# Kernel tuning notes

Measured on AMD Instinct MI355X. Metric: run time of the kernel, lower is better.

Reference implementation:

```python
import jax, jax.numpy as jnp
import numpy as np

N_NODES = 100000


def gcn_conv(x, edge_index, W, b, n_nodes):
    # GCNConv: out = D^{-1/2} (A + I) D^{-1/2} X W + b  (add_self_loops=True)
    xw = x @ W  # [N, F_out]
    loop = jnp.arange(n_nodes, dtype=edge_index.dtype)
    row = jnp.concatenate([edge_index[0], loop])  # source
    col = jnp.concatenate([edge_index[1], loop])  # target
    ones = jnp.ones(row.shape[0], dtype=x.dtype)
    deg = jax.ops.segment_sum(ones, col, num_segments=n_nodes)
    dinv = jnp.where(deg > 0, jax.lax.rsqrt(deg), 0.0)
    norm = dinv[row] * dinv[col]  # [E+N]
    msgs = norm[:, None] * xw[row]  # gather + scale
    out = jax.ops.segment_sum(msgs, col, num_segments=n_nodes)  # scatter-add
    return out + b


def setup_inputs() -> dict:
    key = jax.random.key(0)
    k1, k2, k3, k4 = jax.random.split(key, 4)
    x = jax.random.normal(k1, (N_NODES, 512), dtype=jnp.float32)
    edge_index = jax.random.randint(k2, (2, 3200000), 0, N_NODES, dtype=jnp.int64)
    W1 = jax.random.normal(k3, (512, 16), dtype=jnp.float32) * (1.0 / np.sqrt(512))
    b1 = jnp.zeros((16,), dtype=jnp.float32)
    W2 = jax.random.normal(k4, (16, 7), dtype=jnp.float32) * (1.0 / np.sqrt(16))
    b2 = jnp.zeros((7,), dtype=jnp.float32)
    return {"x": x, "edge_index": edge_index, "W1": W1, "b1": b1, "W2": W2, "b2": b2}


def reference(x, edge_index, W1, b1, W2, b2):
    n = x.shape[0]
    h = gcn_conv(x, edge_index, W1, b1, n)
    h = jax.nn.relu(h)
    # F.dropout(training=self.training) is identity in eval mode
    h = gcn_conv(h, edge_index, W2, b2, n)
    return jax.nn.log_softmax(h, axis=1)
```

## Files before the change

### kernel.cpp

```cpp
#include <hip/hip_runtime.h>
#include <math.h>
#include <stdint.h>

#define NBMAX 512
#define BCAP 10240

__device__ __forceinline__ unsigned int f2bf(float f) {
    unsigned int u = __float_as_uint(f);
    return (u + 0x7FFFu + ((u >> 16) & 1u)) >> 16;
}
__device__ __forceinline__ float bl(unsigned int u) { return __uint_as_float(u << 16); }
__device__ __forceinline__ float bh(unsigned int u) { return __uint_as_float(u & 0xFFFF0000u); }

__global__ void k_zero(int* __restrict__ p, int n) {
    int i = threadIdx.x;
    if (i < n) p[i] = 0;
}

__global__ __launch_bounds__(256) void k_hist_gemm(
    const int* __restrict__ col, int* __restrict__ bucketCnt, int E, int hB, int NB,
    const float* __restrict__ x, const float* __restrict__ W1,
    float* __restrict__ xw, int n) {
    __shared__ float4 sW[2048];
    __shared__ int histL[NBMAX];
    if (blockIdx.x < hB) {
        for (int t = threadIdx.x; t < NB; t += 256) histL[t] = 0;
        __syncthreads();
        int base = blockIdx.x * 4096;
#pragma unroll
        for (int i = 0; i < 16; ++i) {
            int e = base + threadIdx.x + i * 256;
            if (e < E) atomicAdd(&histL[col[e] >> 8], 1);
        }
        __syncthreads();
        for (int t = threadIdx.x; t < NB; t += 256) {
            int c = histL[t];
            if (c) atomicAdd(&bucketCnt[t], c);
        }
        return;
    }
    const float4* w4 = (const float4*)W1;
    for (int p = threadIdx.x; p < 2048; p += 256) sW[p] = w4[p];
    __syncthreads();

    int idx  = (blockIdx.x - hB) * 256 + threadIdx.x;
    int node = idx >> 2, q = idx & 3;
    if (node >= n) return;

    const float4* xr = (const float4*)(x + (size_t)node * 512);
    float ax = 0.f, ay = 0.f, az = 0.f, aw = 0.f;
#pragma unroll 4
    for (int kk = 0; kk < 128; ++kk) {
        float4 xv  = xr[kk];
        float4 w0  = sW[(4 * kk + 0) * 4 + q];
        float4 w1v = sW[(4 * kk + 1) * 4 + q];
        float4 w2v = sW[(4 * kk + 2) * 4 + q];
        float4 w3v = sW[(4 * kk + 3) * 4 + q];
        ax = fmaf(xv.x, w0.x, ax);  ay = fmaf(xv.x, w0.y, ay);
        az = fmaf(xv.x, w0.z, az);  aw = fmaf(xv.x, w0.w, aw);
        ax = fmaf(xv.y, w1v.x, ax); ay = fmaf(xv.y, w1v.y, ay);
        az = fmaf(xv.y, w1v.z, az); aw = fmaf(xv.y, w1v.w, aw);
        ax = fmaf(xv.z, w2v.x, ax); ay = fmaf(xv.z, w2v.y, ay);
        az = fmaf(xv.z, w2v.z, az); aw = fmaf(xv.z, w2v.w, aw);
        ax = fmaf(xv.w, w3v.x, ax); ay = fmaf(xv.w, w3v.y, ay);
        az = fmaf(xv.w, w3v.z, az); aw = fmaf(xv.w, w3v.w, aw);
    }
    float4 r; r.x = ax; r.y = ay; r.z = az; r.w = aw;
    ((float4*)xw)[idx] = r;
}

__global__ void k_scanB(const int* __restrict__ bucketCnt, int* __restrict__ baseB,
                        int* __restrict__ cursor, int* __restrict__ offs,
                        int NB, int N, int E) {
    __shared__ int s[512];
    int t = threadIdx.x;
    int c = (t < NB) ? bucketCnt[t] : 0;
    s[t] = c;
    __syncthreads();
    for (int o = 1; o < 512; o <<= 1) {
        int v = (t >= o) ? s[t - o] : 0;
        __syncthreads();
        s[t] += v;
        __syncthreads();
    }
    if (t < NB) { int ex = s[t] - c; baseB[t] = ex; cursor[t] = ex; }
    if (t == NB) baseB[NB] = E;
    if (t == 0) offs[N] = E;
}

__global__ __launch_bounds__(512) void k_bucket(
    const int* __restrict__ row, const int* __restrict__ col,
    int* __restrict__ cursor, unsigned int* __restrict__ sortedG, int E, int NB) {
    __shared__ int histL[NBMAX];
    __shared__ int offsL[NBMAX];
    __shared__ int gbL[NBMAX];
    __shared__ int sbuf[512];
    __shared__ unsigned int stageW[4096];
    __shared__ unsigned short stageB[4096];
    int t = threadIdx.x;
    for (int i = t; i < NB; i += 512) histL[i] = 0;
    __syncthreads();
    int off = blockIdx.x * 4096;
    unsigned int w[8]; int bk[8]; int rk[8];
#pragma unroll
    for (int i = 0; i < 8; ++i) {
        int e = off + t + i * 512;
        if (e < E) {
            int c = col[e], r = row[e];
            w[i]  = ((unsigned int)r << 8) | (unsigned int)(c & 255);
            bk[i] = c >> 8;
            rk[i] = atomicAdd(&histL[bk[i]], 1);
        } else bk[i] = -1;
    }
    __syncthreads();
    int cnt = (t < NB) ? histL[t] : 0;
    sbuf[t] = cnt;
    __syncthreads();
    for (int o = 1; o < 512; o <<= 1) {
        int v = (t >= o) ? sbuf[t - o] : 0;
        __syncthreads();
        sbuf[t] += v;
        __syncthreads();
    }
    if (t < NB) {
        offsL[t] = sbuf[t] - cnt;
        gbL[t]   = cnt ? atomicAdd(&cursor[t], cnt) : 0;
    }
    __syncthreads();
#pragma unroll
    for (int i = 0; i < 8; ++i) {
        if (bk[i] >= 0) {
            int s2 = offsL[bk[i]] + rk[i];
            stageW[s2] = w[i];
            stageB[s2] = (unsigned short)bk[i];
        }
    }
    __syncthreads();
    int total = min(4096, E - off);
    for (int s2 = t; s2 < total; s2 += 512) {
        int b = stageB[s2];
        sortedG[gbL[b] + (s2 - offsL[b])] = stageW[s2];
    }
}

__global__ __launch_bounds__(512) void k_sortscale(
    unsigned int* __restrict__ sortedG, const int* __restrict__ baseB,
    int* __restrict__ offs, float* __restrict__ dinv,
    const float* __restrict__ xw, unsigned int* __restrict__ sxwh, int N) {
    __shared__ unsigned int wv[BCAP];
    __shared__ int hist[256];
    __shared__ int off_[256];
    __shared__ int sc[256];
    __shared__ float ds[256];
    int t = threadIdx.x, b = blockIdx.x;
    if (t < 256) hist[t] = 0;
    __syncthreads();
    int beg = baseB[b], end = baseB[b + 1];
    int cnt = end - beg;
    for (int i = t; i < cnt; i += 512) {
        unsigned int w = sortedG[beg + i];
        wv[i] = w;
        atomicAdd(&hist[w & 255], 1);
    }
    __syncthreads();
    if (t < 256) sc[t] = hist[t];
    __syncthreads();
    for (int o = 1; o < 256; o <<= 1) {
        int v = 0;
        if (t < 256 && t >= o) v = sc[t - o];
        __syncthreads();
        if (t < 256) sc[t] += v;
        __syncthreads();
    }
    if (t < 256) {
        off_[t] = sc[t] - hist[t];
        int node = b * 256 + t;
        float dv = rsqrtf((float)(hist[t] + 1));
        ds[t] = dv;
        if (node < N) { offs[node] = beg + off_[t]; dinv[node] = dv; }
        hist[t] = 0;
    }
    __syncthreads();
    for (int i = t; i < cnt; i += 512) {
        unsigned int w = wv[i];
        int c = w & 255;
        int r2 = atomicAdd(&hist[c], 1);
        sortedG[beg + off_[c] + r2] = w >> 8;
    }
    const float4* xw4 = (const float4*)xw;
    uint2* dsth = (uint2*)sxwh;
#pragma unroll
    for (int k = 0; k < 2; ++k) {
        int idx = t + k * 512;
        int nl  = idx >> 2;
        int node = b * 256 + nl;
        if (node < N) {
            float s = ds[nl];
            float4 v = xw4[(size_t)b * 1024 + idx];
            unsigned int u0 = f2bf(v.x * s), u1 = f2bf(v.y * s);
            unsigned int u2 = f2bf(v.z * s), u3 = f2bf(v.w * s);
            uint2 o; o.x = u0 | (u1 << 16); o.y = u2 | (u3 << 16);
            dsth[(size_t)b * 1024 + idx] = o;
        }
    }
}

__global__ __launch_bounds__(256) void k_gather1f(
    const int* __restrict__ offs, const int* __restrict__ srow,
    const uint4* __restrict__ s4, const float* __restrict__ dinv,
    const float* __restrict__ W2, const float* __restrict__ b1,
    float* __restrict__ sxw2p, int N) {
    __shared__ float sW2[112];
    __shared__ float sb1[16];
    if (threadIdx.x < 112) sW2[threadIdx.x] = W2[threadIdx.x];
    if (threadIdx.x < 16) sb1[threadIdx.x] = b1[threadIdx.x];
    __syncthreads();
    int idx = blockIdx.x * 256 + threadIdx.x;
    int node = idx >> 1, q = idx & 1;
    if (node >= N) return;
    int beg = offs[node], end = offs[node + 1];

    uint4 sv = s4[(size_t)node * 2 + q];
    float a0 = bl(sv.x), a1 = bh(sv.x), a2 = bl(sv.y), a3 = bh(sv.y);
    float a4 = bl(sv.z), a5 = bh(sv.z), a6 = bl(sv.w), a7 = bh(sv.w);
    int j = beg;
    for (; j + 3 < end; j += 4) {
        int r0 = srow[j], r1 = srow[j + 1], r2 = srow[j + 2], r3 = srow[j + 3];
        uint4 v0 = s4[(size_t)r0 * 2 + q];
        uint4 v1 = s4[(size_t)r1 * 2 + q];
        uint4 v2 = s4[(size_t)r2 * 2 + q];
        uint4 v3 = s4[(size_t)r3 * 2 + q];
        a0 += (bl(v0.x) + bl(v1.x)) + (bl(v2.x) + bl(v3.x));
        a1 += (bh(v0.x) + bh(v1.x)) + (bh(v2.x) + bh(v3.x));
        a2 += (bl(v0.y) + bl(v1.y)) + (bl(v2.y) + bl(v3.y));
        a3 += (bh(v0.y) + bh(v1.y)) + (bh(v2.y) + bh(v3.y));
        a4 += (bl(v0.z) + bl(v1.z)) + (bl(v2.z) + bl(v3.z));
        a5 += (bh(v0.z) + bh(v1.z)) + (bh(v2.z) + bh(v3.z));
        a6 += (bl(v0.w) + bl(v1.w)) + (bl(v2.w) + bl(v3.w));
        a7 += (bh(v0.w) + bh(v1.w)) + (bh(v2.w) + bh(v3.w));
    }
    for (; j < end; ++j) {
        int r = srow[j];
        uint4 v = s4[(size_t)r * 2 + q];
        a0 += bl(v.x); a1 += bh(v.x); a2 += bl(v.y); a3 += bh(v.y);
        a4 += bl(v.z); a5 += bh(v.z); a6 += bl(v.w); a7 += bh(v.w);
    }
    float d = dinv[node];
    float h[8];
    h[0] = fmaxf(fmaf(d, a0, sb1[q * 8 + 0]), 0.f);
    h[1] = fmaxf(fmaf(d, a1, sb1[q * 8 + 1]), 0.f);
    h[2] = fmaxf(fmaf(d, a2, sb1[q * 8 + 2]), 0.f);
    h[3] = fmaxf(fmaf(d, a3, sb1[q * 8 + 3]), 0.f);
    h[4] = fmaxf(fmaf(d, a4, sb1[q * 8 + 4]), 0.f);
    h[5] = fmaxf(fmaf(d, a5, sb1[q * 8 + 5]), 0.f);
    h[6] = fmaxf(fmaf(d, a6, sb1[q * 8 + 6]), 0.f);
    h[7] = fmaxf(fmaf(d, a7, sb1[q * 8 + 7]), 0.f);
    float o[7] = {0.f, 0.f, 0.f, 0.f, 0.f, 0.f, 0.f};
    int rbase = q * 8;
#pragma unroll
    for (int i = 0; i < 8; ++i) {
        float hv = h[i];
#pragma unroll
        for (int jj = 0; jj < 7; ++jj) o[jj] = fmaf(hv, sW2[(rbase + i) * 7 + jj], o[jj]);
    }
#pragma unroll
    for (int jj = 0; jj < 7; ++jj) o[jj] += __shfl_xor(o[jj], 1, 64);
    float4 wv4;
    if (q == 0) { wv4.x = o[0] * d; wv4.y = o[1] * d; wv4.z = o[2] * d; wv4.w = o[3] * d; }
    else        { wv4.x = o[4] * d; wv4.y = o[5] * d; wv4.z = o[6] * d; wv4.w = 0.f; }
    ((float4*)sxw2p)[(size_t)node * 2 + q] = wv4;
}

__global__ __launch_bounds__(256) void k_gather2f(
    const int* __restrict__ offs, const int* __restrict__ srow,
    const float* __restrict__ sxw2p, const float* __restrict__ dinv,
    const float* __restrict__ b2, float* __restrict__ out, int N) {
    __shared__ float sb2[8];
    if (threadIdx.x < 7) sb2[threadIdx.x] = b2[threadIdx.x];
    if (threadIdx.x == 7) sb2[7] = 0.f;
    __syncthreads();
    int idx = blockIdx.x * 256 + threadIdx.x;
    int node = idx >> 1, q = idx & 1;
    if (node >= N) return;
    int beg = offs[node], end = offs[node + 1];
    const float4* s4 = (const float4*)sxw2p;
    float4 a = s4[(size_t)node * 2 + q];
    int j = beg;
    for (; j + 3 < end; j += 4) {
        int r0 = srow[j], r1 = srow[j + 1], r2 = srow[j + 2], r3 = srow[j + 3];
        float4 v0 = s4[(size_t)r0 * 2 + q];
        float4 v1 = s4[(size_t)r1 * 2 + q];
        float4 v2 = s4[(size_t)r2 * 2 + q];
        float4 v3 = s4[(size_t)r3 * 2 + q];
        a.x += (v0.x + v1.x) + (v2.x + v3.x);
        a.y += (v0.y + v1.y) + (v2.y + v3.y);
        a.z += (v0.z + v1.z) + (v2.z + v3.z);
        a.w += (v0.w + v1.w) + (v2.w + v3.w);
    }
    for (; j < end; ++j) {
        int r = srow[j];
        float4 v = s4[(size_t)r * 2 + q];
        a.x += v.x; a.y += v.y; a.z += v.z; a.w += v.w;
    }
    float d = dinv[node];
    float z0 = fmaf(d, a.x, sb2[q * 4 + 0]);
    float z1 = fmaf(d, a.y, sb2[q * 4 + 1]);
    float z2 = fmaf(d, a.z, sb2[q * 4 + 2]);
    float z3 = (q == 0) ? fmaf(d, a.w, sb2[3]) : -INFINITY;
    float m = fmaxf(fmaxf(z0, z1), fmaxf(z2, z3));
    m = fmaxf(m, __shfl_xor(m, 1, 64));
    float s = expf(z0 - m) + expf(z1 - m) + expf(z2 - m) + ((q == 0) ? expf(z3 - m) : 0.f);
    s += __shfl_xor(s, 1, 64);
    float l = m + logf(s);
    float* ob = out + (size_t)node * 7;
    if (q == 0) { ob[0] = z0 - l; ob[1] = z1 - l; ob[2] = z2 - l; ob[3] = z3 - l; }
    else        { ob[4] = z0 - l; ob[5] = z1 - l; ob[6] = z2 - l; }
}

extern "C" void kernel_launch(void* const* d_in, const int* in_sizes, int n_in,
                              void* d_out, int out_size, void* d_ws, size_t ws_size,
                              hipStream_t stream) {
    const float* x  = (const float*)d_in[0];
    const int*   ei = (const int*)d_in[1];
    const float* W1 = (const float*)d_in[2];
    const float* b1 = (const float*)d_in[3];
    const float* W2 = (const float*)d_in[4];
    const float* b2 = (const float*)d_in[5];

    int N = in_sizes[0] / 512;
    int E = in_sizes[1] / 2;
    const int* row = ei;
    const int* col = ei + E;

    int NB = (N + 255) >> 8;

    int* bucketCnt = (int*)d_ws;
    int* baseB     = bucketCnt + 512;
    int* cursor    = baseB + 512;
    int* offs      = cursor + 512;
    unsigned int* sortedG = (unsigned int*)(offs + ((N + 4) & ~3));
    float* dinv  = (float*)(sortedG + E);
    float* xw1   = dinv + N;
    unsigned int* sxwh = (unsigned int*)(xw1 + (size_t)16 * N);
    float* sxw2p = xw1;
    float* out   = (float*)d_out;

    int hB = (E + 4095) / 4096;
    int gG = (4 * N + 255) / 256;
    int bB = (E + 4095) / 4096;
    int gP = (2 * N + 255) / 256;

    k_zero     <<<1, 512, 0, stream>>>(bucketCnt, NB);
    k_hist_gemm<<<hB + gG, 256, 0, stream>>>(col, bucketCnt, E, hB, NB, x, W1, xw1, N);
    k_scanB    <<<1, 512, 0, stream>>>(bucketCnt, baseB, cursor, offs, NB, N, E);
    k_bucket   <<<bB, 512, 0, stream>>>(row, col, cursor, sortedG, E, NB);
    k_sortscale<<<NB, 512, 0, stream>>>(sortedG, baseB, offs, dinv, xw1, sxwh, N);
    k_gather1f <<<gP, 256, 0, stream>>>(offs, (const int*)sortedG, (const uint4*)sxwh,
                                        dinv, W2, b1, sxw2p, N);
    k_gather2f <<<gP, 256, 0, stream>>>(offs, (const int*)sortedG, sxw2p, dinv, b2, out, N);
}
```

Measured before the change: 458.9 us.

## Reorder gather nodes by in-degree to balance wavefront work

Builds an in-degree histogram in the sort kernel, scans it, and writes a permutation that groups nodes by degree bin. Both gather kernels then process nodes in that order, so the lanes of a wavefront have similar loop trip counts and less divergence. The cost is two extra small kernel launches, an extra indirection load per thread, and scattered output and node-feature accesses because neighbouring threads no longer handle neighbouring nodes.

```diff
diff --git a/kernel.cpp b/kernel.cpp
--- a/kernel.cpp
+++ b/kernel.cpp
@@ -4,6 +4,7 @@
 
 #define NBMAX 512
 #define BCAP 10240
+#define DBINS 128
 
 __device__ __forceinline__ unsigned int f2bf(float f) {
     unsigned int u = __float_as_uint(f);
@@ -13,7 +14,7 @@
 __device__ __forceinline__ float bh(unsigned int u) { return __uint_as_float(u & 0xFFFF0000u); }
 
 __global__ void k_zero(int* __restrict__ p, int n) {
-    int i = threadIdx.x;
+    int i = blockIdx.x * 512 + threadIdx.x;
     if (i < n) p[i] = 0;
 }
 
@@ -146,14 +147,17 @@
 __global__ __launch_bounds__(512) void k_sortscale(
     unsigned int* __restrict__ sortedG, const int* __restrict__ baseB,
     int* __restrict__ offs, float* __restrict__ dinv,
-    const float* __restrict__ xw, unsigned int* __restrict__ sxwh, int N) {
+    const float* __restrict__ xw, unsigned int* __restrict__ sxwh,
+    int* __restrict__ degHist, int N) {
     __shared__ unsigned int wv[BCAP];
     __shared__ int hist[256];
     __shared__ int off_[256];
     __shared__ int sc[256];
     __shared__ float ds[256];
+    __shared__ int dh[DBINS];
     int t = threadIdx.x, b = blockIdx.x;
     if (t < 256) hist[t] = 0;
+    if (t >= 256 && t < 256 + DBINS) dh[t - 256] = 0;
     __syncthreads();
     int beg = baseB[b], end = baseB[b + 1];
     int cnt = end - beg;
@@ -175,12 +179,18 @@
     if (t < 256) {
         off_[t] = sc[t] - hist[t];
         int node = b * 256 + t;
-        float dv = rsqrtf((float)(hist[t] + 1));
+        int degv = hist[t];
+        float dv = rsqrtf((float)(degv + 1));
         ds[t] = dv;
-        if (node < N) { offs[node] = beg + off_[t]; dinv[node] = dv; }
+        if (node < N) {
+            offs[node] = beg + off_[t];
+            dinv[node] = dv;
+            atomicAdd(&dh[min(degv, DBINS - 1)], 1);
+        }
         hist[t] = 0;
     }
     __syncthreads();
+    if (t < DBINS && dh[t]) atomicAdd(&degHist[t], dh[t]);
     for (int i = t; i < cnt; i += 512) {
         unsigned int w = wv[i];
         int c = w & 255;
@@ -205,10 +215,48 @@
     }
 }
 
+__global__ void k_permscan(const int* __restrict__ degHist, int* __restrict__ degCur) {
+    __shared__ int s[DBINS];
+    int t = threadIdx.x;
+    int c = degHist[t];
+    s[t] = c;
+    __syncthreads();
+    for (int o = 1; o < DBINS; o <<= 1) {
+        int v = (t >= o) ? s[t - o] : 0;
+        __syncthreads();
+        s[t] += v;
+        __syncthreads();
+    }
+    degCur[t] = s[t] - c;
+}
+
+__global__ __launch_bounds__(256) void k_perm(
+    const int* __restrict__ offs, int* __restrict__ degCur,
+    int* __restrict__ perm, int N) {
+    __shared__ int lh[DBINS];
+    __shared__ int gb[DBINS];
+    int t = threadIdx.x;
+    if (t < DBINS) lh[t] = 0;
+    __syncthreads();
+    int node = blockIdx.x * 256 + t;
+    int bin = 0, r = 0;
+    bool ok = node < N;
+    if (ok) {
+        int d = offs[node + 1] - offs[node];
+        bin = min(d, DBINS - 1);
+        r = atomicAdd(&lh[bin], 1);
+    }
+    __syncthreads();
+    if (t < DBINS && lh[t]) gb[t] = atomicAdd(&degCur[t], lh[t]);
+    __syncthreads();
+    if (ok) perm[gb[bin] + r] = node;
+}
+
 __global__ __launch_bounds__(256) void k_gather1f(
     const int* __restrict__ offs, const int* __restrict__ srow,
     const uint4* __restrict__ s4, const float* __restrict__ dinv,
     const float* __restrict__ W2, const float* __restrict__ b1,
+    const int* __restrict__ perm,
     float* __restrict__ sxw2p, int N) {
     __shared__ float sW2[112];
     __shared__ float sb1[16];
@@ -216,8 +264,9 @@
     if (threadIdx.x < 16) sb1[threadIdx.x] = b1[threadIdx.x];
     __syncthreads();
     int idx = blockIdx.x * 256 + threadIdx.x;
-    int node = idx >> 1, q = idx & 1;
-    if (node >= N) return;
+    int m = idx >> 1, q = idx & 1;
+    if (m >= N) return;
+    int node = perm[m];
     int beg = offs[node], end = offs[node + 1];
 
     uint4 sv = s4[(size_t)node * 2 + q];
@@ -274,14 +323,16 @@
 __global__ __launch_bounds__(256) void k_gather2f(
     const int* __restrict__ offs, const int* __restrict__ srow,
     const float* __restrict__ sxw2p, const float* __restrict__ dinv,
-    const float* __restrict__ b2, float* __restrict__ out, int N) {
+    const float* __restrict__ b2, const int* __restrict__ perm,
+    float* __restrict__ out, int N) {
     __shared__ float sb2[8];
     if (threadIdx.x < 7) sb2[threadIdx.x] = b2[threadIdx.x];
     if (threadIdx.x == 7) sb2[7] = 0.f;
     __syncthreads();
     int idx = blockIdx.x * 256 + threadIdx.x;
-    int node = idx >> 1, q = idx & 1;
-    if (node >= N) return;
+    int m = idx >> 1, q = idx & 1;
+    if (m >= N) return;
+    int node = perm[m];
     int beg = offs[node], end = offs[node + 1];
     const float4* s4 = (const float4*)sxw2p;
     float4 a = s4[(size_t)node * 2 + q];
@@ -307,11 +358,11 @@
     float z1 = fmaf(d, a.y, sb2[q * 4 + 1]);
     float z2 = fmaf(d, a.z, sb2[q * 4 + 2]);
     float z3 = (q == 0) ? fmaf(d, a.w, sb2[3]) : -INFINITY;
-    float m = fmaxf(fmaxf(z0, z1), fmaxf(z2, z3));
-    m = fmaxf(m, __shfl_xor(m, 1, 64));
-    float s = expf(z0 - m) + expf(z1 - m) + expf(z2 - m) + ((q == 0) ? expf(z3 - m) : 0.f);
+    float m2 = fmaxf(fmaxf(z0, z1), fmaxf(z2, z3));
+    m2 = fmaxf(m2, __shfl_xor(m2, 1, 64));
+    float s = expf(z0 - m2) + expf(z1 - m2) + expf(z2 - m2) + ((q == 0) ? expf(z3 - m2) : 0.f);
     s += __shfl_xor(s, 1, 64);
-    float l = m + logf(s);
+    float l = m2 + logf(s);
     float* ob = out + (size_t)node * 7;
     if (q == 0) { ob[0] = z0 - l; ob[1] = z1 - l; ob[2] = z2 - l; ob[3] = z3 - l; }
     else        { ob[4] = z0 - l; ob[5] = z1 - l; ob[6] = z2 - l; }
@@ -337,11 +388,14 @@
     int* bucketCnt = (int*)d_ws;
     int* baseB     = bucketCnt + 512;
     int* cursor    = baseB + 512;
-    int* offs      = cursor + 512;
+    int* degHist   = cursor + 512;
+    int* degCur    = degHist + 128;
+    int* offs      = degCur + 128;
     unsigned int* sortedG = (unsigned int*)(offs + ((N + 4) & ~3));
     float* dinv  = (float*)(sortedG + E);
     float* xw1   = dinv + N;
     unsigned int* sxwh = (unsigned int*)(xw1 + (size_t)16 * N);
+    int* perm    = (int*)(sxwh + (size_t)8 * N);
     float* sxw2p = xw1;
     float* out   = (float*)d_out;
 
@@ -349,13 +403,16 @@
     int gG = (4 * N + 255) / 256;
     int bB = (E + 4095) / 4096;
     int gP = (2 * N + 255) / 256;
-
-    k_zero     <<<1, 512, 0, stream>>>(bucketCnt, NB);
+    int zN = 512 * 3 + 256;
+
+    k_zero     <<<(zN + 511) / 512, 512, 0, stream>>>(bucketCnt, zN);
     k_hist_gemm<<<hB + gG, 256, 0, stream>>>(col, bucketCnt, E, hB, NB, x, W1, xw1, N);
     k_scanB    <<<1, 512, 0, stream>>>(bucketCnt, baseB, cursor, offs, NB, N, E);
     k_bucket   <<<bB, 512, 0, stream>>>(row, col, cursor, sortedG, E, NB);
-    k_sortscale<<<NB, 512, 0, stream>>>(sortedG, baseB, offs, dinv, xw1, sxwh, N);
+    k_sortscale<<<NB, 512, 0, stream>>>(sortedG, baseB, offs, dinv, xw1, sxwh, degHist, N);
+    k_permscan <<<1, DBINS, 0, stream>>>(degHist, degCur);
+    k_perm     <<<NB, 256, 0, stream>>>(offs, degCur, perm, N);
     k_gather1f <<<gP, 256, 0, stream>>>(offs, (const int*)sortedG, (const uint4*)sxwh,
-                                        dinv, W2, b1, sxw2p, N);
-    k_gather2f <<<gP, 256, 0, stream>>>(offs, (const int*)sortedG, sxw2p, dinv, b2, out, N);
-}
+                                        dinv, W2, b1, perm, sxw2p, N);
+    k_gather2f <<<gP, 256, 0, stream>>>(offs, (const int*)sortedG, sxw2p, dinv, b2, perm, out, N);
+}
```

After: 481.1 us. 1.05x slower.

## Compute first-layer GEMM with bf16x3 split MFMA instead of scalar FMA

Applied to the files above, without the earlier changes.

Replaces the per-thread scalar FP32 FMA loop for x@W1 with MFMA 16x16x32 bf16 instructions. Both operands are split into high and low bf16 parts and three MFMAs are summed to approximate FP32 accuracy. W1 is pre-split into LDS, which shares a union with the histogram buffer. The GEMM reads 200MB of x and was likely memory-bound, so the gain depends on how much the FMA issue rate was limiting. The split trades a small accuracy loss for fewer ALU cycles.

```diff
diff --git a/kernel.cpp b/kernel.cpp
--- a/kernel.cpp
+++ b/kernel.cpp
@@ -4,6 +4,9 @@
 
 #define NBMAX 512
 #define BCAP 10240
+
+typedef __attribute__((ext_vector_type(8))) short short8;
+typedef __attribute__((ext_vector_type(4))) float f32x4;
 
 __device__ __forceinline__ unsigned int f2bf(float f) {
     unsigned int u = __float_as_uint(f);
@@ -21,52 +24,85 @@
     const int* __restrict__ col, int* __restrict__ bucketCnt, int E, int hB, int NB,
     const float* __restrict__ x, const float* __restrict__ W1,
     float* __restrict__ xw, int n) {
-    __shared__ float4 sW[2048];
-    __shared__ int histL[NBMAX];
+    __shared__ union {
+        int hist[NBMAX];
+        struct { uint4 bhi[1024]; uint4 blo[1024]; } g;
+    } sh;
     if (blockIdx.x < hB) {
-        for (int t = threadIdx.x; t < NB; t += 256) histL[t] = 0;
+        for (int t = threadIdx.x; t < NB; t += 256) sh.hist[t] = 0;
         __syncthreads();
         int base = blockIdx.x * 4096;
 #pragma unroll
         for (int i = 0; i < 16; ++i) {
             int e = base + threadIdx.x + i * 256;
-            if (e < E) atomicAdd(&histL[col[e] >> 8], 1);
+            if (e < E) atomicAdd(&sh.hist[col[e] >> 8], 1);
         }
         __syncthreads();
         for (int t = threadIdx.x; t < NB; t += 256) {
-            int c = histL[t];
+            int c = sh.hist[t];
             if (c) atomicAdd(&bucketCnt[t], c);
         }
         return;
     }
-    const float4* w4 = (const float4*)W1;
-    for (int p = threadIdx.x; p < 2048; p += 256) sW[p] = w4[p];
-    __syncthreads();
-
-    int idx  = (blockIdx.x - hB) * 256 + threadIdx.x;
-    int node = idx >> 2, q = idx & 3;
-    if (node >= n) return;
-
-    const float4* xr = (const float4*)(x + (size_t)node * 512);
-    float ax = 0.f, ay = 0.f, az = 0.f, aw = 0.f;
-#pragma unroll 4
-    for (int kk = 0; kk < 128; ++kk) {
-        float4 xv  = xr[kk];
-        float4 w0  = sW[(4 * kk + 0) * 4 + q];
-        float4 w1v = sW[(4 * kk + 1) * 4 + q];
-        float4 w2v = sW[(4 * kk + 2) * 4 + q];
-        float4 w3v = sW[(4 * kk + 3) * 4 + q];
-        ax = fmaf(xv.x, w0.x, ax);  ay = fmaf(xv.x, w0.y, ay);
-        az = fmaf(xv.x, w0.z, az);  aw = fmaf(xv.x, w0.w, aw);
-        ax = fmaf(xv.y, w1v.x, ax); ay = fmaf(xv.y, w1v.y, ay);
-        az = fmaf(xv.y, w1v.z, az); aw = fmaf(xv.y, w1v.w, aw);
-        ax = fmaf(xv.z, w2v.x, ax); ay = fmaf(xv.z, w2v.y, ay);
-        az = fmaf(xv.z, w2v.z, az); aw = fmaf(xv.z, w2v.w, aw);
-        ax = fmaf(xv.w, w3v.x, ax); ay = fmaf(xv.w, w3v.y, ay);
-        az = fmaf(xv.w, w3v.z, az); aw = fmaf(xv.w, w3v.w, aw);
-    }
-    float4 r; r.x = ax; r.y = ay; r.z = az; r.w = aw;
-    ((float4*)xw)[idx] = r;
+    for (int s = threadIdx.x; s < 1024; s += 256) {
+        int ts = s >> 6, l = s & 63;
+        int colc = l & 15, kg = l >> 4;
+        int kbase = ts * 32 + kg * 8;
+        unsigned int hw[8], lw[8];
+#pragma unroll
+        for (int j = 0; j < 8; ++j) {
+            float wv = W1[(size_t)(kbase + j) * 16 + colc];
+            unsigned int u = __float_as_uint(wv);
+            unsigned int h = u >> 16;
+            unsigned int lo = f2bf(wv - bl(h));
+            hw[j] = h; lw[j] = lo;
+        }
+        uint4 ph, pl;
+        ph.x = hw[0] | (hw[1] << 16); ph.y = hw[2] | (hw[3] << 16);
+        ph.z = hw[4] | (hw[5] << 16); ph.w = hw[6] | (hw[7] << 16);
+        pl.x = lw[0] | (lw[1] << 16); pl.y = lw[2] | (lw[3] << 16);
+        pl.z = lw[4] | (lw[5] << 16); pl.w = lw[6] | (lw[7] << 16);
+        sh.g.bhi[s] = ph; sh.g.blo[s] = pl;
+    }
+    __syncthreads();
+
+    int w = threadIdx.x >> 6, lane = threadIdx.x & 63;
+    int mtMax = (n + 15) >> 4;
+    int mt = (blockIdx.x - hB) * 4 + w;
+    if (mt >= mtMax) return;
+    int rowbase = mt * 16;
+    int r0 = rowbase + (lane & 15);
+    if (r0 >= n) r0 = n - 1;
+    int kg = lane >> 4;
+    const float4* xr = (const float4*)(x + (size_t)r0 * 512);
+    f32x4 acc = {0.f, 0.f, 0.f, 0.f};
+#pragma unroll 2
+    for (int ts = 0; ts < 16; ++ts) {
+        float4 u = xr[ts * 8 + kg * 2];
+        float4 v = xr[ts * 8 + kg * 2 + 1];
+        float e[8] = {u.x, u.y, u.z, u.w, v.x, v.y, v.z, v.w};
+        short8 ah, al;
+#pragma unroll
+        for (int j = 0; j < 8; ++j) {
+            unsigned int uu = __float_as_uint(e[j]);
+            unsigned int h = uu >> 16;
+            unsigned int lo = f2bf(e[j] - bl(h));
+            ah[j] = (short)h;
+            al[j] = (short)lo;
+        }
+        uint4 bhw = sh.g.bhi[ts * 64 + lane];
+        uint4 blw = sh.g.blo[ts * 64 + lane];
+        short8 bhv = *reinterpret_cast<const short8*>(&bhw);
+        short8 blv = *reinterpret_cast<const short8*>(&blw);
+        acc = __builtin_amdgcn_mfma_f32_16x16x32_bf16(ah, bhv, acc, 0, 0, 0);
+        acc = __builtin_amdgcn_mfma_f32_16x16x32_bf16(al, bhv, acc, 0, 0, 0);
+        acc = __builtin_amdgcn_mfma_f32_16x16x32_bf16(ah, blv, acc, 0, 0, 0);
+    }
+#pragma unroll
+    for (int r = 0; r < 4; ++r) {
+        int orow = rowbase + kg * 4 + r;
+        if (orow < n) xw[(size_t)orow * 16 + (lane & 15)] = acc[r];
+    }
 }
 
 __global__ void k_scanB(const int* __restrict__ bucketCnt, int* __restrict__ baseB,
@@ -346,12 +382,13 @@
     float* out   = (float*)d_out;
 
     int hB = (E + 4095) / 4096;
-    int gG = (4 * N + 255) / 256;
+    int mtMax = (N + 15) / 16;
+    int gM = (mtMax + 3) / 4;
     int bB = (E + 4095) / 4096;
     int gP = (2 * N + 255) / 256;
 
     k_zero     <<<1, 512, 0, stream>>>(bucketCnt, NB);
-    k_hist_gemm<<<hB + gG, 256, 0, stream>>>(col, bucketCnt, E, hB, NB, x, W1, xw1, N);
+    k_hist_gemm<<<hB + gM, 256, 0, stream>>>(col, bucketCnt, E, hB, NB, x, W1, xw1, N);
     k_scanB    <<<1, 512, 0, stream>>>(bucketCnt, baseB, cursor, offs, NB, N, E);
     k_bucket   <<<bB, 512, 0, stream>>>(row, col, cursor, sortedG, E, NB);
     k_sortscale<<<NB, 512, 0, stream>>>(sortedG, baseB, offs, dinv, xw1, sxwh, N);
```

After: 448.4 us. 1.02x faster.
